# Kernel optimization log

Hardware: AMD Instinct MI355X
Metric: run time of the kernel (lower is better)

Reference implementation:

```python
import jax, jax.numpy as jnp
import numpy as np

D_QK = 64

def _xavier(key, shape):
    # matches nn.init.xavier_uniform_ on (H, fan_in, fan_out)
    fan_in, fan_out = shape[-2], shape[-1]
    limit = float(np.sqrt(6.0 / (fan_in + fan_out)))
    return jax.random.uniform(key, shape, jnp.float32, -limit, limit)

def setup_inputs() -> dict:
    key = jax.random.key(0)
    kx, kq, kk, kv = jax.random.split(key, 4)
    B, M, d_model, H, d_QK, d_V = 4, 2048, 1024, 16, 64, 64
    x = jax.random.normal(kx, (B, M, d_model), jnp.float32)
    W_Q = _xavier(kq, (H, d_model, d_QK))
    W_K = _xavier(kk, (H, d_model, d_QK))
    W_V = _xavier(kv, (H, d_model, d_V))
    return {"x": x, "W_Q": W_Q, "W_K": W_K, "W_V": W_V}

def reference(x, W_Q, W_K, W_V):
    B, M, N = x.shape
    H = W_Q.shape[0]
    # per-head projections: [B,H,M,d]
    Q = jnp.einsum('bmn,hnd->bhmd', x, W_Q)
    K = jnp.einsum('bmn,hnd->bhmd', x, W_K)
    V = jnp.einsum('bmn,hnd->bhmd', x, W_V)
    scale = 1.0 / jnp.sqrt(jnp.asarray(D_QK, x.dtype))
    attn = jax.nn.softmax(jnp.einsum('bhmd,bhkd->bhmk', Q, K) * scale, axis=-1)
    out = jnp.einsum('bhmk,bhkd->bhmd', attn, V)  # [B,H,M,d_V]
    # transpose heads next to d_V and concat: [B,M,H*d_V] == [B,M,N]
    return out.transpose(0, 2, 1, 3).reshape(B, M, N)
```

## Files before the change

kernel.cpp:

```cpp
#include <hip/hip_runtime.h>

typedef __attribute__((ext_vector_type(8))) _Float16 f16x8;
typedef __attribute__((ext_vector_type(2))) __fp16 fp16v2;
typedef __attribute__((ext_vector_type(4))) float f32x4;
typedef _Float16 f16;
typedef unsigned short u16;
typedef unsigned int u32;

#define DEV __device__ __forceinline__

DEV u32 packh2(float a, float b) {
  union { f16 h[2]; u32 u; } x;
  x.h[0] = (f16)a; x.h[1] = (f16)b;
  return x.u;
}
DEV u32 pkrtz(float a, float b) {
  union { fp16v2 h; u32 u; } x;
  x.h = __builtin_amdgcn_cvt_pkrtz(a, b);
  return x.u;
}
DEV float exp2_fast(float x) {
  float r;
  asm("v_exp_f32 %0, %1" : "=v"(r) : "v"(x));
  return r;
}

typedef __attribute__((address_space(1))) const u32 ASG_u32;
typedef __attribute__((address_space(3))) u32 ASL_u32;
DEV void gload16(const void* g, void* l) {
  __builtin_amdgcn_global_load_lds((ASG_u32*)g, (ASL_u32*)l, 16, 0, 0);
}

__global__ __launch_bounds__(256) void k_half_x(const float* __restrict__ x,
                                                f16* __restrict__ xh) {
  const size_t i = ((size_t)blockIdx.x * 256 + threadIdx.x) * 8;
  float4 a = *(const float4*)(x + i);
  float4 c = *(const float4*)(x + i + 4);
  uint4 u;
  u.x = packh2(a.x, a.y); u.y = packh2(a.z, a.w);
  u.z = packh2(c.x, c.y); u.w = packh2(c.z, c.w);
  *(uint4*)(xh + i) = u;
}

__global__ __launch_bounds__(256) void k_prep_w(const float* __restrict__ Wq,
                                                const float* __restrict__ Wk,
                                                const float* __restrict__ Wv,
                                                f16* __restrict__ wt) {
  __shared__ float tile[64][65];
  const int bx = blockIdx.x;
  const int w = bx >> 8;
  const int rem = bx & 255;
  const int h = rem >> 4;
  const int nc = rem & 15;
  const float* W = (w == 0) ? Wq : ((w == 1) ? Wk : Wv);
  const int t = threadIdx.x;

  {
    const int r = t >> 2;
    const int cc = (t & 3) * 16;
    const float* src = W + ((size_t)h * 1024 + nc * 64 + r) * 64 + cc;
#pragma unroll
    for (int j = 0; j < 4; ++j) {
      float4 v = *(const float4*)(src + j * 4);
      tile[r][cc + j * 4 + 0] = v.x;
      tile[r][cc + j * 4 + 1] = v.y;
      tile[r][cc + j * 4 + 2] = v.z;
      tile[r][cc + j * 4 + 3] = v.w;
    }
  }
  __syncthreads();
  {
    const int d = t >> 2;
    const int n0 = (t & 3) * 16;
    const size_t base = ((size_t)(w * 16 + h) * 64 + d) * 1024 + nc * 64 + n0;
    uint4 u0, u1;
    u0.x = packh2(tile[n0 + 0][d], tile[n0 + 1][d]);
    u0.y = packh2(tile[n0 + 2][d], tile[n0 + 3][d]);
    u0.z = packh2(tile[n0 + 4][d], tile[n0 + 5][d]);
    u0.w = packh2(tile[n0 + 6][d], tile[n0 + 7][d]);
    u1.x = packh2(tile[n0 + 8][d], tile[n0 + 9][d]);
    u1.y = packh2(tile[n0 + 10][d], tile[n0 + 11][d]);
    u1.z = packh2(tile[n0 + 12][d], tile[n0 + 13][d]);
    u1.w = packh2(tile[n0 + 14][d], tile[n0 + 15][d]);
    *(uint4*)(wt + base) = u0;
    *(uint4*)(wt + base + 8) = u1;
  }
}

__global__ __launch_bounds__(256, 4) void k_proj(
    const f16* __restrict__ xh, const f16* __restrict__ wt,
    f16* __restrict__ Q, f16* __restrict__ K, f16* __restrict__ Vt) {
  __shared__ __align__(16) char ldsb[32768];
  int bid = blockIdx.x;
  bid = (bid & 7) * 192 + (bid >> 3);
  const int bm = bid / 24;
  const int bn = bid % 24;
  const int w = bn >> 3;
  const int hp = bn & 7;
  const int wrow = w * 1024 + hp * 128;
  const bool isV = (w == 2);
  const int t = threadIdx.x;
  const int wave = t >> 6;
  const int lane = t & 63;
  const int l15 = lane & 15;
  const int wr = wave >> 1;
  const int wc = wave & 1;

  f32x4 acc[4][4];
#pragma unroll
  for (int mi = 0; mi < 4; ++mi)
#pragma unroll
    for (int ni = 0; ni < 4; ++ni) acc[mi][ni] = (f32x4)(0.0f);

  for (int kt = 0; kt < 16; ++kt) {
    const int k0 = kt * 64;
#pragma unroll
    for (int i = 0; i < 4; ++i) {
      const int ci = wave * 4 + i;
      const int row = ci * 8 + (lane >> 3);
      const int cb = ((lane & 7) * 16) ^ ((row & 7) << 4);
      const size_t ga = ((size_t)(bm * 128 + row) * 1024 + k0) * 2;
      gload16((const char*)xh + ga + cb, ldsb + ci * 1024);
      const size_t gb = ((size_t)(wrow + row) * 1024 + k0) * 2;
      gload16((const char*)wt + gb + cb, ldsb + 16384 + ci * 1024);
    }
    __syncthreads();

#pragma unroll
    for (int ks = 0; ks < 2; ++ks) {
      f16x8 af[4], bfr[4];
#pragma unroll
      for (int mi = 0; mi < 4; ++mi) {
        const int row = wr * 64 + mi * 16 + l15;
        const int cb = (((lane >> 4) * 16) + ks * 64) ^ ((row & 7) << 4);
        af[mi] = *(const f16x8*)(ldsb + row * 128 + cb);
      }
#pragma unroll
      for (int ni = 0; ni < 4; ++ni) {
        const int row = wc * 64 + ni * 16 + l15;
        const int cb = (((lane >> 4) * 16) + ks * 64) ^ ((row & 7) << 4);
        bfr[ni] = *(const f16x8*)(ldsb + 16384 + row * 128 + cb);
      }
#pragma unroll
      for (int mi = 0; mi < 4; ++mi)
#pragma unroll
        for (int ni = 0; ni < 4; ++ni)
          acc[mi][ni] = __builtin_amdgcn_mfma_f32_16x16x32_f16(af[mi], bfr[ni], acc[mi][ni], 0, 0, 0);
    }
    __syncthreads();
  }

  const int rb = bm * 128 + wr * 64;
#pragma unroll
  for (int mi = 0; mi < 4; ++mi) {
#pragma unroll
    for (int ni = 0; ni < 4; ++ni) {
      f32x4 v = acc[mi][ni];
      const int dl = wc * 64 + ni * 16 + l15;
      const int hh = hp * 2 + (dl >> 6);
      const int d = dl & 63;
      const int m0 = rb + mi * 16 + ((lane >> 4) << 2);
      const int b = m0 >> 11;
      const int ml = m0 & 2047;
      if (isV) {
        uint2 u;
        u.x = packh2(v[0], v[1]);
        u.y = packh2(v[2], v[3]);
        *(uint2*)(Vt + ((size_t)((b * 16 + hh) * 64 + d)) * 2048 + ml) = u;
      } else {
        const float sc = (w == 0) ? 0.18033688f : 1.0f;
        f16* A = (w == 0) ? Q : K;
#pragma unroll
        for (int j = 0; j < 4; ++j)
          A[((size_t)(b * 16 + hh) * 2048 + (ml + j)) * 64 + d] = (f16)(v[j] * sc);
      }
    }
  }
}

__global__ __launch_bounds__(512, 4) void k_attn(
    const f16* __restrict__ Q, const f16* __restrict__ K,
    const f16* __restrict__ Vt, float* __restrict__ out) {
  __shared__ __align__(16) char ldsb[65536];
  const int raw = blockIdx.x;
  const int bh = (raw & 7) * 8 + (raw >> 6);
  const int qt = (raw >> 3) & 7;
  const int b = bh >> 4;
  const int h = bh & 15;
  const int t = threadIdx.x;
  const int wave = t >> 6;
  const int lane = t & 63;
  const int l15 = lane & 15;
  const int g = lane >> 4;
  char* sP = ldsb + 32768 + wave * 4096;

  f16x8 qf[2][2];
  const size_t qbase = ((size_t)bh * 2048 + qt * 256 + wave * 32) * 64;
#pragma unroll
  for (int mf = 0; mf < 2; ++mf)
#pragma unroll
    for (int ks = 0; ks < 2; ++ks) {
      const size_t off = qbase + (size_t)(mf * 16 + l15) * 64 + ks * 32 + g * 8;
      qf[mf][ks] = *(const f16x8*)(Q + off);
    }

  f32x4 o[2][4];
  float ms[2], ls[2];
#pragma unroll
  for (int mf = 0; mf < 2; ++mf) { ms[mf] = -1e30f; ls[mf] = 0.0f; }
#pragma unroll
  for (int mf = 0; mf < 2; ++mf)
#pragma unroll
    for (int df = 0; df < 4; ++df) o[mf][df] = (f32x4)(0.0f);

  const size_t kvbase = (size_t)bh * 2048 * 64;

  const int srow = wave * 8 + (lane >> 3);
  const int scb0 = ((lane & 7) * 16) ^ (((lane >> 3) & 7) << 4);

#pragma unroll 1
  for (int kt = 0; kt < 33; ++kt) {
    if (kt < 32) {
      char* dst = ldsb + (kt & 1) * 16384;
      const size_t gk = (kvbase + (size_t)(kt * 64 + srow) * 64) * 2;
      gload16((const char*)K + gk + scb0, dst + wave * 1024);
      const size_t gv = (kvbase + (size_t)srow * 2048 + kt * 64) * 2;
      gload16((const char*)Vt + gv + scb0, dst + 8192 + wave * 1024);
    }
    if (kt == 0) { __syncthreads(); continue; }
    const char* kb = ldsb + ((kt - 1) & 1) * 16384;
    const char* vbuf = kb + 8192;

    f32x4 st[2][4];
#pragma unroll
    for (int mf = 0; mf < 2; ++mf)
#pragma unroll
      for (int nf = 0; nf < 4; ++nf) st[mf][nf] = (f32x4)(0.0f);
#pragma unroll
    for (int ks = 0; ks < 2; ++ks) {
      f16x8 kf[4];
#pragma unroll
      for (int nf = 0; nf < 4; ++nf) {
        const int row = nf * 16 + l15;
        const int cb = ((g * 16) + ks * 64) ^ ((row & 7) << 4);
        kf[nf] = *(const f16x8*)(kb + row * 128 + cb);
      }
#pragma unroll
      for (int mf = 0; mf < 2; ++mf)
#pragma unroll
        for (int nf = 0; nf < 4; ++nf)
          st[mf][nf] = __builtin_amdgcn_mfma_f32_16x16x32_f16(kf[nf], qf[mf][ks], st[mf][nf], 0, 0, 0);
    }

#pragma unroll
    for (int mf = 0; mf < 2; ++mf) {
      float rm = fmaxf(fmaxf(fmaxf(st[mf][0][0], st[mf][0][1]), fmaxf(st[mf][0][2], st[mf][0][3])),
                       fmaxf(fmaxf(st[mf][1][0], st[mf][1][1]), fmaxf(st[mf][1][2], st[mf][1][3])));
      rm = fmaxf(rm, fmaxf(fmaxf(fmaxf(st[mf][2][0], st[mf][2][1]), fmaxf(st[mf][2][2], st[mf][2][3])),
                           fmaxf(fmaxf(st[mf][3][0], st[mf][3][1]), fmaxf(st[mf][3][2], st[mf][3][3]))));
      rm = fmaxf(rm, __shfl_xor(rm, 16));
      rm = fmaxf(rm, __shfl_xor(rm, 32));
      if (__any(rm > ms[mf] + 11.5f)) {
        const float mnew = fmaxf(ms[mf], rm);
        const float alpha = exp2_fast(ms[mf] - mnew);
        ms[mf] = mnew;
        ls[mf] *= alpha;
        f32x4 av;
#pragma unroll
        for (int j = 0; j < 4; ++j) av[j] = __shfl(alpha, g * 4 + j);
#pragma unroll
        for (int df = 0; df < 4; ++df) o[mf][df] *= av;
      }
      const float m = ms[mf];
      float p[4][4], part = 0.0f;
#pragma unroll
      for (int nf = 0; nf < 4; ++nf) {
#pragma unroll
        for (int j = 0; j < 4; ++j) {
          p[nf][j] = exp2_fast(st[mf][nf][j] - m);
          part += p[nf][j];
        }
      }
      ls[mf] += part;
      const int prow = mf * 16 + l15;
      char* pr = sP + prow * 128;
      const int swz = (prow & 7) << 4;
#pragma unroll
      for (int nf = 0; nf < 4; ++nf) {
        uint2 u;
        u.x = pkrtz(p[nf][0], p[nf][1]);
        u.y = pkrtz(p[nf][2], p[nf][3]);
        *(uint2*)(pr + (((nf << 5) + (g << 3)) ^ swz)) = u;
      }
    }
    asm volatile("" ::: "memory");

#pragma unroll
    for (int ks = 0; ks < 2; ++ks) {
      f16x8 pa[2];
#pragma unroll
      for (int mf = 0; mf < 2; ++mf) {
        const int prow = mf * 16 + l15;
        pa[mf] = *(const f16x8*)(sP + prow * 128 + ((ks * 64 + g * 16) ^ ((prow & 7) << 4)));
      }
#pragma unroll
      for (int df = 0; df < 4; ++df) {
        const int row = df * 16 + l15;
        const int cb = ((g * 16) + ks * 64) ^ ((row & 7) << 4);
        const f16x8 vb = *(const f16x8*)(vbuf + row * 128 + cb);
#pragma unroll
        for (int mf = 0; mf < 2; ++mf)
          o[mf][df] = __builtin_amdgcn_mfma_f32_16x16x32_f16(pa[mf], vb, o[mf][df], 0, 0, 0);
      }
    }
    __syncthreads();
  }

#pragma unroll
  for (int mf = 0; mf < 2; ++mf) {
    float l = ls[mf];
    l += __shfl_xor(l, 16);
    l += __shfl_xor(l, 32);
    const float inv = 1.0f / l;
    f32x4 iv;
#pragma unroll
    for (int j = 0; j < 4; ++j) iv[j] = __shfl(inv, g * 4 + j);
#pragma unroll
    for (int j = 0; j < 4; ++j) {
      const int m = qt * 256 + wave * 32 + mf * 16 + g * 4 + j;
#pragma unroll
      for (int df = 0; df < 4; ++df) {
        const int d = df * 16 + l15;
        out[((size_t)(b * 2048 + m)) * 1024 + h * 64 + d] = o[mf][df][j] * iv[j];
      }
    }
  }
}

extern "C" void kernel_launch(void* const* d_in, const int* in_sizes, int n_in,
                              void* d_out, int out_size, void* d_ws, size_t ws_size,
                              hipStream_t stream) {
  (void)in_sizes; (void)n_in; (void)out_size; (void)ws_size;
  const float* x  = (const float*)d_in[0];
  const float* Wq = (const float*)d_in[1];
  const float* Wk = (const float*)d_in[2];
  const float* Wv = (const float*)d_in[3];
  float* out = (float*)d_out;

  f16* ws = (f16*)d_ws;
  f16* xh = ws + 0;
  f16* wt = ws + 8388608;
  f16* Q  = ws + 11534336;
  f16* K  = ws + 19922944;
  f16* Vt = ws + 28311552;

  k_half_x<<<4096, 256, 0, stream>>>(x, xh);
  k_prep_w<<<768, 256, 0, stream>>>(Wq, Wk, Wv, wt);
  k_proj<<<1536, 256, 0, stream>>>(xh, wt, Q, K, Vt);
  k_attn<<<512, 512, 0, stream>>>(Q, K, Vt, out);
}
```

Before: 182.7 us.

## Switch attention kernel to 32x32x16 MFMA with register-shuffled P operand

Recasts the QK^T and PV matrix products in the attention kernel from 16x16x32 MFMA tiles to 32x32x16 tiles, so each lane owns a full query column. The P matrix is no longer staged through shared memory. Instead the fp16 pairs are exchanged between half-waves with cross-lane shuffles to form the PV A-operand. This removes the per-wave LDS P buffer and halves the shared allocation, cutting LDS write/read traffic and possibly raising occupancy. In exchange it adds shuffle instructions and larger per-lane accumulator vectors, which raise register pressure.

```diff
diff --git a/kernel.cpp b/kernel.cpp
--- a/kernel.cpp
+++ b/kernel.cpp
@@ -3,6 +3,7 @@
 typedef __attribute__((ext_vector_type(8))) _Float16 f16x8;
 typedef __attribute__((ext_vector_type(2))) __fp16 fp16v2;
 typedef __attribute__((ext_vector_type(4))) float f32x4;
+typedef __attribute__((ext_vector_type(16))) float f32x16;
 typedef _Float16 f16;
 typedef unsigned short u16;
 typedef unsigned int u32;
@@ -181,7 +182,7 @@
 __global__ __launch_bounds__(512, 4) void k_attn(
     const f16* __restrict__ Q, const f16* __restrict__ K,
     const f16* __restrict__ Vt, float* __restrict__ out) {
-  __shared__ __align__(16) char ldsb[65536];
+  __shared__ __align__(16) char ldsb[32768];
   const int raw = blockIdx.x;
   const int bh = (raw & 7) * 8 + (raw >> 6);
   const int qt = (raw >> 3) & 7;
@@ -190,28 +191,19 @@
   const int t = threadIdx.x;
   const int wave = t >> 6;
   const int lane = t & 63;
-  const int l15 = lane & 15;
-  const int g = lane >> 4;
-  char* sP = ldsb + 32768 + wave * 4096;
-
-  f16x8 qf[2][2];
-  const size_t qbase = ((size_t)bh * 2048 + qt * 256 + wave * 32) * 64;
-#pragma unroll
-  for (int mf = 0; mf < 2; ++mf)
-#pragma unroll
-    for (int ks = 0; ks < 2; ++ks) {
-      const size_t off = qbase + (size_t)(mf * 16 + l15) * 64 + ks * 32 + g * 8;
-      qf[mf][ks] = *(const f16x8*)(Q + off);
-    }
-
-  f32x4 o[2][4];
-  float ms[2], ls[2];
-#pragma unroll
-  for (int mf = 0; mf < 2; ++mf) { ms[mf] = -1e30f; ls[mf] = 0.0f; }
-#pragma unroll
-  for (int mf = 0; mf < 2; ++mf)
-#pragma unroll
-    for (int df = 0; df < 4; ++df) o[mf][df] = (f32x4)(0.0f);
+  const int l31 = lane & 31;
+  const int hh = lane >> 5;
+
+  f16x8 qf[4];
+  const int q0 = qt * 256 + wave * 32;
+  const size_t qrow = ((size_t)bh * 2048 + q0 + l31) * 64 + hh * 8;
+#pragma unroll
+  for (int c = 0; c < 4; ++c) qf[c] = *(const f16x8*)(Q + qrow + c * 16);
+
+  f32x16 od[2];
+  od[0] = (f32x16)(0.0f);
+  od[1] = (f32x16)(0.0f);
+  float ms = -1e30f, ls = 0.0f;
 
   const size_t kvbase = (size_t)bh * 2048 * 64;
 
@@ -231,109 +223,98 @@
     const char* kb = ldsb + ((kt - 1) & 1) * 16384;
     const char* vbuf = kb + 8192;
 
-    f32x4 st[2][4];
-#pragma unroll
-    for (int mf = 0; mf < 2; ++mf)
-#pragma unroll
-      for (int nf = 0; nf < 4; ++nf) st[mf][nf] = (f32x4)(0.0f);
-#pragma unroll
-    for (int ks = 0; ks < 2; ++ks) {
-      f16x8 kf[4];
-#pragma unroll
-      for (int nf = 0; nf < 4; ++nf) {
-        const int row = nf * 16 + l15;
-        const int cb = ((g * 16) + ks * 64) ^ ((row & 7) << 4);
-        kf[nf] = *(const f16x8*)(kb + row * 128 + cb);
-      }
-#pragma unroll
-      for (int mf = 0; mf < 2; ++mf)
-#pragma unroll
-        for (int nf = 0; nf < 4; ++nf)
-          st[mf][nf] = __builtin_amdgcn_mfma_f32_16x16x32_f16(kf[nf], qf[mf][ks], st[mf][nf], 0, 0, 0);
-    }
-
-#pragma unroll
-    for (int mf = 0; mf < 2; ++mf) {
-      float rm = fmaxf(fmaxf(fmaxf(st[mf][0][0], st[mf][0][1]), fmaxf(st[mf][0][2], st[mf][0][3])),
-                       fmaxf(fmaxf(st[mf][1][0], st[mf][1][1]), fmaxf(st[mf][1][2], st[mf][1][3])));
-      rm = fmaxf(rm, fmaxf(fmaxf(fmaxf(st[mf][2][0], st[mf][2][1]), fmaxf(st[mf][2][2], st[mf][2][3])),
-                           fmaxf(fmaxf(st[mf][3][0], st[mf][3][1]), fmaxf(st[mf][3][2], st[mf][3][3]))));
-      rm = fmaxf(rm, __shfl_xor(rm, 16));
-      rm = fmaxf(rm, __shfl_xor(rm, 32));
-      if (__any(rm > ms[mf] + 11.5f)) {
-        const float mnew = fmaxf(ms[mf], rm);
-        const float alpha = exp2_fast(ms[mf] - mnew);
-        ms[mf] = mnew;
-        ls[mf] *= alpha;
-        f32x4 av;
-#pragma unroll
-        for (int j = 0; j < 4; ++j) av[j] = __shfl(alpha, g * 4 + j);
-#pragma unroll
-        for (int df = 0; df < 4; ++df) o[mf][df] *= av;
-      }
-      const float m = ms[mf];
-      float p[4][4], part = 0.0f;
-#pragma unroll
-      for (int nf = 0; nf < 4; ++nf) {
-#pragma unroll
-        for (int j = 0; j < 4; ++j) {
-          p[nf][j] = exp2_fast(st[mf][nf][j] - m);
-          part += p[nf][j];
-        }
-      }
-      ls[mf] += part;
-      const int prow = mf * 16 + l15;
-      char* pr = sP + prow * 128;
-      const int swz = (prow & 7) << 4;
-#pragma unroll
-      for (int nf = 0; nf < 4; ++nf) {
-        uint2 u;
-        u.x = pkrtz(p[nf][0], p[nf][1]);
-        u.y = pkrtz(p[nf][2], p[nf][3]);
-        *(uint2*)(pr + (((nf << 5) + (g << 3)) ^ swz)) = u;
-      }
-    }
-    asm volatile("" ::: "memory");
-
-#pragma unroll
-    for (int ks = 0; ks < 2; ++ks) {
-      f16x8 pa[2];
-#pragma unroll
-      for (int mf = 0; mf < 2; ++mf) {
-        const int prow = mf * 16 + l15;
-        pa[mf] = *(const f16x8*)(sP + prow * 128 + ((ks * 64 + g * 16) ^ ((prow & 7) << 4)));
-      }
-#pragma unroll
-      for (int df = 0; df < 4; ++df) {
-        const int row = df * 16 + l15;
-        const int cb = ((g * 16) + ks * 64) ^ ((row & 7) << 4);
+    f32x16 st[2];
+    st[0] = (f32x16)(0.0f);
+    st[1] = (f32x16)(0.0f);
+#pragma unroll
+    for (int c = 0; c < 4; ++c) {
+#pragma unroll
+      for (int tt = 0; tt < 2; ++tt) {
+        const int row = tt * 32 + l31;
+        const int cb = (c * 32 + hh * 16) ^ ((row & 7) << 4);
+        const f16x8 kf = *(const f16x8*)(kb + row * 128 + cb);
+        st[tt] = __builtin_amdgcn_mfma_f32_32x32x16_f16(kf, qf[c], st[tt], 0, 0, 0);
+      }
+    }
+
+    float rm = fmaxf(fmaxf(fmaxf(st[0][0], st[0][1]), fmaxf(st[0][2], st[0][3])),
+                     fmaxf(fmaxf(st[0][4], st[0][5]), fmaxf(st[0][6], st[0][7])));
+    rm = fmaxf(rm, fmaxf(fmaxf(fmaxf(st[0][8], st[0][9]), fmaxf(st[0][10], st[0][11])),
+                         fmaxf(fmaxf(st[0][12], st[0][13]), fmaxf(st[0][14], st[0][15]))));
+    float rm1 = fmaxf(fmaxf(fmaxf(st[1][0], st[1][1]), fmaxf(st[1][2], st[1][3])),
+                      fmaxf(fmaxf(st[1][4], st[1][5]), fmaxf(st[1][6], st[1][7])));
+    rm1 = fmaxf(rm1, fmaxf(fmaxf(fmaxf(st[1][8], st[1][9]), fmaxf(st[1][10], st[1][11])),
+                           fmaxf(fmaxf(st[1][12], st[1][13]), fmaxf(st[1][14], st[1][15]))));
+    rm = fmaxf(rm, rm1);
+    rm = fmaxf(rm, __shfl_xor(rm, 32));
+    if (__any(rm > ms + 11.5f)) {
+      const float mnew = fmaxf(ms, rm);
+      const float alpha = exp2_fast(ms - mnew);
+      ms = mnew;
+      ls *= alpha;
+      float av[16];
+#pragma unroll
+      for (int r = 0; r < 16; ++r) av[r] = __shfl(alpha, (r & 3) + 8 * (r >> 2) + 4 * hh);
+#pragma unroll
+      for (int r = 0; r < 16; ++r) { od[0][r] *= av[r]; od[1][r] *= av[r]; }
+    }
+    float p[2][16];
+    float part = 0.0f;
+#pragma unroll
+    for (int tt = 0; tt < 2; ++tt)
+#pragma unroll
+      for (int r = 0; r < 16; ++r) {
+        p[tt][r] = exp2_fast(st[tt][r] - ms);
+        part += p[tt][r];
+      }
+    ls += part;
+
+    union { u32 u[4]; f16x8 v; } pa[4];
+#pragma unroll
+    for (int tt = 0; tt < 2; ++tt) {
+#pragma unroll
+      for (int cp = 0; cp < 2; ++cp) {
+        const int ro = 8 * cp + 4 * hh;
+        const int rs = 8 * cp + 4 * (1 - hh);
+        const u32 own0 = pkrtz(p[tt][ro], p[tt][ro + 1]);
+        const u32 own1 = pkrtz(p[tt][ro + 2], p[tt][ro + 3]);
+        const u32 snd0 = pkrtz(p[tt][rs], p[tt][rs + 1]);
+        const u32 snd1 = pkrtz(p[tt][rs + 2], p[tt][rs + 3]);
+        const u32 rcv0 = (u32)__shfl_xor((int)snd0, 32);
+        const u32 rcv1 = (u32)__shfl_xor((int)snd1, 32);
+        const int c = 2 * tt + cp;
+        pa[c].u[0] = hh ? rcv0 : own0;
+        pa[c].u[1] = hh ? rcv1 : own1;
+        pa[c].u[2] = hh ? own0 : rcv0;
+        pa[c].u[3] = hh ? own1 : rcv1;
+      }
+    }
+
+#pragma unroll
+    for (int c = 0; c < 4; ++c) {
+#pragma unroll
+      for (int dt = 0; dt < 2; ++dt) {
+        const int row = dt * 32 + l31;
+        const int cb = (c * 32 + hh * 16) ^ ((row & 7) << 4);
         const f16x8 vb = *(const f16x8*)(vbuf + row * 128 + cb);
-#pragma unroll
-        for (int mf = 0; mf < 2; ++mf)
-          o[mf][df] = __builtin_amdgcn_mfma_f32_16x16x32_f16(pa[mf], vb, o[mf][df], 0, 0, 0);
+        od[dt] = __builtin_amdgcn_mfma_f32_32x32x16_f16(pa[c].v, vb, od[dt], 0, 0, 0);
       }
     }
     __syncthreads();
   }
 
-#pragma unroll
-  for (int mf = 0; mf < 2; ++mf) {
-    float l = ls[mf];
-    l += __shfl_xor(l, 16);
-    l += __shfl_xor(l, 32);
-    const float inv = 1.0f / l;
-    f32x4 iv;
-#pragma unroll
-    for (int j = 0; j < 4; ++j) iv[j] = __shfl(inv, g * 4 + j);
-#pragma unroll
-    for (int j = 0; j < 4; ++j) {
-      const int m = qt * 256 + wave * 32 + mf * 16 + g * 4 + j;
-#pragma unroll
-      for (int df = 0; df < 4; ++df) {
-        const int d = df * 16 + l15;
-        out[((size_t)(b * 2048 + m)) * 1024 + h * 64 + d] = o[mf][df][j] * iv[j];
-      }
-    }
+  float l = ls + __shfl_xor(ls, 32);
+  const float inv = 1.0f / l;
+  float iv[16];
+#pragma unroll
+  for (int r = 0; r < 16; ++r) iv[r] = __shfl(inv, (r & 3) + 8 * (r >> 2) + 4 * hh);
+#pragma unroll
+  for (int r = 0; r < 16; ++r) {
+    const int q = (r & 3) + 8 * (r >> 2) + 4 * hh;
+    const int m = q0 + q;
+    const size_t base = ((size_t)(b * 2048 + m)) * 1024 + h * 64 + l31;
+    out[base] = od[0][r] * iv[r];
+    out[base + 32] = od[1][r] * iv[r];
   }
 }
 
```

Measured after the change: 620.8 us. 240% more time.
